# Performance work log

Measured on AMD Instinct MI355X. Metric: run time of the kernel, lower is better.

The kernel has to match this reference:

```python
import jax, jax.numpy as jnp
import numpy as np

NUM_HEADS = 6


def dwconv_tokens(tokens, H, W, w, b, stride):
    # tokens: (B, N, C) -> depthwise conv in (B, C, H, W) -> (B, N', C)
    B, N, C = tokens.shape
    x = tokens.transpose(0, 2, 1).reshape(B, C, H, W)
    y = jax.lax.conv_general_dilated(
        x, w, window_strides=(stride, stride), padding=[(1, 1), (1, 1)],
        feature_group_count=C, dimension_numbers=('NCHW', 'OIHW', 'NCHW'))
    y = y + b[None, :, None, None]
    Bc, Cc, Hs, Ws = y.shape
    return y.reshape(Bc, Cc, Hs * Ws).transpose(0, 2, 1), Hs, Ws


def neg_softmax(a):
    # sign(x) * softmax(|x|) along last axis
    return jnp.sign(a) * jax.nn.softmax(jnp.abs(a), axis=-1)


def split_heads(t, nh):
    B, N, C = t.shape
    return t.reshape(B, N, nh, C // nh).transpose(0, 2, 1, 3)  # (B, H, N, d)


def setup_inputs() -> dict:
    key = jax.random.key(0)
    ks = jax.random.split(key, 16)
    B, H, W, C = 8, 56, 56, 384
    N = H * W
    s = 0.02
    inp = {
        'x': jax.random.normal(ks[0], (B, N, C), jnp.float32),
        'H': H, 'W': W,
        'q_w': jax.random.normal(ks[1], (C, C), jnp.float32) * s,
        'q_b': jax.random.normal(ks[2], (C,), jnp.float32) * s,
        'k_w': jax.random.normal(ks[3], (C, C), jnp.float32) * s,
        'k_b': jax.random.normal(ks[4], (C,), jnp.float32) * s,
        'v_w': jax.random.normal(ks[5], (C, C), jnp.float32) * s,
        'v_b': jax.random.normal(ks[6], (C,), jnp.float32) * s,
        'q_dw_w': jax.random.normal(ks[7], (C, 1, 3, 3), jnp.float32) * 0.1,
        'q_dw_b': jax.random.normal(ks[8], (C,), jnp.float32) * s,
        'k_dw_w': jax.random.normal(ks[9], (C, 1, 3, 3), jnp.float32) * 0.1,
        'k_dw_b': jax.random.normal(ks[10], (C,), jnp.float32) * s,
        'v_dw_w': jax.random.normal(ks[11], (C, 1, 3, 3), jnp.float32) * 0.1,
        'v_dw_b': jax.random.normal(ks[12], (C,), jnp.float32) * s,
        'proj_w': jax.random.normal(ks[13], (C, C), jnp.float32) * s,
        'proj_b': jax.random.normal(ks[14], (C,), jnp.float32) * s,
    }
    return inp


def reference(x, H, W, q_w, q_b, k_w, k_b, v_w, v_b,
              q_dw_w, q_dw_b, k_dw_w, k_dw_b, v_dw_w, v_dw_b,
              proj_w, proj_b):
    B, N, C = x.shape
    nh = NUM_HEADS
    hd = C // nh
    scale = hd ** -0.5
    # linear q/k/v (torch Linear: x @ W.T + b)
    q = x @ q_w.T + q_b
    k = x @ k_w.T + k_b
    v = x @ v_w.T + v_b
    # depthwise conv projections (q: stride 1, k/v: stride 2)
    q, Hq, Wq = dwconv_tokens(q, H, W, q_dw_w, q_dw_b, 1)
    k, _, _ = dwconv_tokens(k, H, W, k_dw_w, k_dw_b, 2)
    v, _, _ = dwconv_tokens(v, H, W, v_dw_w, v_dw_b, 2)
    q = split_heads(q, nh)  # (B, nh, Nq, hd)
    k = split_heads(k, nh)  # (B, nh, Nk, hd)
    v = split_heads(v, nh)
    attn = jnp.einsum('bhqd,bhkd->bhqk', q, k) * scale
    attn = neg_softmax(attn)
    out = jnp.einsum('bhqk,bhkd->bhqd', attn, v)
    out = out.transpose(0, 2, 1, 3).reshape(B, -1, C)
    out = out @ proj_w.T + proj_b
    return out
```

## Files before the change

kernel.cpp:

```cpp
#include <hip/hip_runtime.h>
#include <hip/hip_bf16.h>
#include <stdint.h>

typedef __attribute__((ext_vector_type(4))) float f32x4;
typedef __attribute__((ext_vector_type(8))) short s16x8;
typedef __attribute__((ext_vector_type(4))) short s16x4;
typedef __attribute__((ext_vector_type(8))) unsigned short u16x8;

#define NB 8
#define HH 56
#define WW0 56
#define NC 384
#define NQTOK (HH*WW0)
#define NKTOK 784
#define NHEAD 6
#define HDIM 64
#define QSCALE 0.18033688f

__device__ __forceinline__ float bf2f(unsigned short u) {
    union { unsigned int i; float f; } x; x.i = ((unsigned int)u) << 16; return x.f;
}
__device__ __forceinline__ unsigned short f2bf(float f) {
    union { float f; unsigned int i; } x; x.f = f;
    unsigned int r = x.i + 0x7FFFu + ((x.i >> 16) & 1u);
    return (unsigned short)(r >> 16);
}
__device__ __forceinline__ unsigned short f2bf_rn(float f) {
    union { float f; unsigned int i; } x; x.f = f;
    return (unsigned short)((x.i + 0x8000u) >> 16);
}

__global__ __launch_bounds__(256) void prep_all(
    const float* __restrict__ x,
    const float* __restrict__ qw, const float* __restrict__ kw,
    const float* __restrict__ vw, const float* __restrict__ pw,
    const float* __restrict__ qb, const float* __restrict__ kb,
    const float* __restrict__ vb, const float* __restrict__ pb,
    const float* __restrict__ qdw, const float* __restrict__ kdw, const float* __restrict__ vdw,
    unsigned short* __restrict__ xbf, unsigned short* __restrict__ wbf,
    float* __restrict__ wtab, float* __restrict__ ball)
{
    const int bid = blockIdx.x;
    const int t = threadIdx.x;
    if (bid < 4704) {
        int i = bid*256 + t;
        f32x4 a0 = *(const f32x4*)&x[(size_t)i*8];
        f32x4 a1 = *(const f32x4*)&x[(size_t)i*8 + 4];
        u16x8 p;
        #pragma unroll
        for (int j = 0; j < 4; ++j) { p[j] = f2bf(a0[j]); p[j+4] = f2bf(a1[j]); }
        *(u16x8*)&xbf[(size_t)i*8] = p;
    } else if (bid < 4992) {
        int i = (bid - 4704)*256 + t;
        int m = i / 18432;
        const float* s = (m==0) ? qw : ((m==1) ? kw : ((m==2) ? vw : pw));
        int r = i - m*18432;
        f32x4 a0 = *(const f32x4*)&s[(size_t)r*8];
        f32x4 a1 = *(const f32x4*)&s[(size_t)r*8 + 4];
        u16x8 p;
        #pragma unroll
        for (int j = 0; j < 4; ++j) { p[j] = f2bf(a0[j]); p[j+4] = f2bf(a1[j]); }
        *(u16x8*)&wbf[(size_t)i*8] = p;
    } else {
        int j = (bid - 4992)*256 + t;
        if (j < 3*9*NC) {
            int m = j / (9*NC); int r = j - m*(9*NC);
            int tap = r / NC; int c = r - tap*NC;
            const float* src = (m==0) ? qdw : ((m==1) ? kdw : vdw);
            wtab[j] = src[c*9 + tap];
        } else {
            int jj = j - 3*9*NC;
            if (jj < 4*NC) {
                int m = jj / NC, r = jj - m*NC;
                ball[jj] = ((m==0) ? qb : ((m==1) ? kb : ((m==2) ? vb : pb)))[r];
            }
        }
    }
}

template<bool OUT_F32>
__global__ __launch_bounds__(512) void gemm_bt_bf(
    const unsigned short* __restrict__ A,
    const unsigned short* __restrict__ Wall,
    const float* __restrict__ Ball,
    unsigned short* __restrict__ Oa, unsigned short* __restrict__ Ob, unsigned short* __restrict__ Oc,
    float* __restrict__ Of,
    int ntiles)
{
    __shared__ unsigned short lA[256*64];
    __shared__ unsigned short lW[128*64];
    char* lAb = (char*)lA;
    char* lWb = (char*)lW;
    const int bid = blockIdx.x;
    const int nt = bid % ntiles;
    const int mt = bid / ntiles;
    const int mat = nt / 3;
    const int ncol = nt - mat*3;
    const unsigned short* W = Wall + (size_t)mat*NC*NC;
    const float* Bsel = Ball + mat*NC;
    unsigned short* Osel = (mat==0) ? Oa : ((mat==1) ? Ob : Oc);
    const int Mbase = mt*256, Nbase = ncol*128;
    const int t = threadIdx.x;
    const int w = t >> 6, l = t & 63;
    const int wr = w >> 1, wc = w & 1;
    const int lr = l & 15, lg = l >> 4;
    const int swg = (lr & 7) << 4;

    f32x4 acc[4][4] = {};
    for (int kt = 0; kt < 6; ++kt) {
        __syncthreads();
        #pragma unroll
        for (int i = 0; i < 4; ++i) {
            int c = i*512 + t;
            int row = c >> 3, c8 = c & 7;
            int sdst = row*128 + ((c8*16) ^ ((row & 7) << 4));
            *(u16x8*)(lAb + sdst) = *(const u16x8*)&A[(size_t)(Mbase+row)*NC + kt*64 + c8*8];
        }
        #pragma unroll
        for (int i = 0; i < 2; ++i) {
            int c = i*512 + t;
            int row = c >> 3, c8 = c & 7;
            int sdst = row*128 + ((c8*16) ^ ((row & 7) << 4));
            *(u16x8*)(lWb + sdst) = *(const u16x8*)&W[(size_t)(Nbase+row)*NC + kt*64 + c8*8];
        }
        __syncthreads();
        #pragma unroll
        for (int kk = 0; kk < 2; ++kk) {
            s16x8 af[4], bfr[4];
            #pragma unroll
            for (int m = 0; m < 4; ++m)
                af[m] = *(const s16x8*)(lAb + (wr*64 + m*16 + lr)*128 + ((kk*64 + lg*16) ^ swg));
            #pragma unroll
            for (int n = 0; n < 4; ++n)
                bfr[n] = *(const s16x8*)(lWb + (wc*64 + n*16 + lr)*128 + ((kk*64 + lg*16) ^ swg));
            #pragma unroll
            for (int m = 0; m < 4; ++m)
                #pragma unroll
                for (int n = 0; n < 4; ++n)
                    acc[m][n] = __builtin_amdgcn_mfma_f32_16x16x32_bf16(af[m], bfr[n], acc[m][n], 0, 0, 0);
        }
    }
    #pragma unroll
    for (int n = 0; n < 4; ++n) {
        int col = Nbase + wc*64 + n*16 + lr;
        float bias = Bsel[col];
        #pragma unroll
        for (int m = 0; m < 4; ++m) {
            int row0 = Mbase + wr*64 + m*16 + lg*4;
            #pragma unroll
            for (int r = 0; r < 4; ++r) {
                float vv = acc[m][n][r] + bias;
                if (OUT_F32) Of[(size_t)(row0 + r)*NC + col] = vv;
                else Osel[(size_t)(row0 + r)*NC + col] = f2bf(vv);
            }
        }
    }
}

template<int S, int HO, int WO, bool SCALE, int MODE>
__device__ __forceinline__ void dwconv_body(
    int idx,
    const unsigned short* __restrict__ in,
    const float* __restrict__ wt9,
    const float* __restrict__ bias,
    unsigned short* __restrict__ outp)
{
    const int nc8 = NC/8;
    int c8 = idx % nc8; int rest = idx / nc8;
    int wo = rest % WO; rest /= WO;
    int ho = rest % HO; int b = rest / HO;
    int c0 = c8*8;
    f32x4 b0 = *(const f32x4*)&bias[c0];
    f32x4 b1 = *(const f32x4*)&bias[c0+4];
    float acc[8];
    #pragma unroll
    for (int j = 0; j < 4; ++j) { acc[j] = b0[j]; acc[j+4] = b1[j]; }
    #pragma unroll
    for (int kh = 0; kh < 3; ++kh) {
        int h = ho*S + kh - 1;
        if (h < 0 || h >= HH) continue;
        #pragma unroll
        for (int kw = 0; kw < 3; ++kw) {
            int ww = wo*S + kw - 1;
            if (ww < 0 || ww >= WW0) continue;
            int tap = kh*3 + kw;
            u16x8 xv = *(const u16x8*)&in[((size_t)b*(HH*WW0) + h*WW0 + ww)*NC + c0];
            f32x4 w0 = *(const f32x4*)&wt9[tap*NC + c0];
            f32x4 w1 = *(const f32x4*)&wt9[tap*NC + c0 + 4];
            #pragma unroll
            for (int j = 0; j < 4; ++j) {
                acc[j]   += bf2f(xv[j])   * w0[j];
                acc[j+4] += bf2f(xv[j+4]) * w1[j];
            }
        }
    }
    if (SCALE) {
        #pragma unroll
        for (int j = 0; j < 8; ++j) acc[j] *= QSCALE;
    }
    int tok = ho*WO + wo;
    int hh = c0 >> 6, d0 = c0 & 63;
    if (MODE == 0) {
        u16x8 ov;
        #pragma unroll
        for (int j = 0; j < 8; ++j) ov[j] = f2bf(acc[j]);
        *(u16x8*)&outp[((size_t)b*(HO*WO) + tok)*NC + c0] = ov;
    } else if (MODE == 1) {
        u16x8 ov;
        #pragma unroll
        for (int j = 0; j < 8; ++j) ov[j] = f2bf(acc[j]);
        *(u16x8*)&outp[((size_t)(b*NHEAD + hh)*(HO*WO) + tok)*HDIM + d0] = ov;
    } else {
        size_t base = ((size_t)(b*NHEAD + hh)*HDIM + d0)*(HO*WO) + tok;
        #pragma unroll
        for (int j = 0; j < 8; ++j)
            outp[base + (size_t)j*(HO*WO)] = f2bf(acc[j]);
    }
}

__global__ __launch_bounds__(256) void dwconv_kv(
    const unsigned short* __restrict__ preK, const unsigned short* __restrict__ preV,
    const float* __restrict__ wtK, const float* __restrict__ wtV,
    const float* __restrict__ biasK, const float* __restrict__ biasV,
    unsigned short* __restrict__ Kpk, unsigned short* __restrict__ Vt)
{
    const int bid = blockIdx.x;
    if (bid < 1176) {
        int idx = bid*256 + threadIdx.x;
        dwconv_body<2,28,28,false,1>(idx, preK, wtK, biasK, Kpk);
    } else {
        int idx = (bid-1176)*256 + threadIdx.x;
        dwconv_body<2,28,28,false,2>(idx, preV, wtV, biasV, Vt);
    }
}

__global__ __launch_bounds__(256) void dwconv_q(
    const unsigned short* __restrict__ in,
    const float* __restrict__ wt9, const float* __restrict__ bias,
    unsigned short* __restrict__ outp)
{
    int idx = blockIdx.x*256 + threadIdx.x;
    dwconv_body<1,56,56,true,0>(idx, in, wt9, bias, outp);
}

__global__ __launch_bounds__(256) void attn_fwd(
    const unsigned short* __restrict__ Q,
    const unsigned short* __restrict__ Kpk,
    const unsigned short* __restrict__ Vt,
    unsigned short* __restrict__ ctx)
{
    __shared__ unsigned short lK[2][4096];
    __shared__ unsigned short lV[2][4096];
    const int bid = blockIdx.x;
    const int xcd = bid & 7, slot = bid >> 3;
    const int bh = xcd*6 + slot/25;
    const int qt = slot % 25;
    const int b = bh / NHEAD, h = bh - b*NHEAD;
    const int t = threadIdx.x;
    const int w = t >> 6, l = t & 63;
    const int lq = l & 15, lg = l >> 4;
    const int wq0 = qt*128 + w*32;
    const int wq0c = (wq0 > NQTOK-32) ? (NQTOK-32) : wq0;

    const unsigned short* Qb = Q + ((size_t)b*NQTOK + wq0c + lq)*NC + h*HDIM;
    s16x8 qA[2][2];
    qA[0][0] = *(const s16x8*)&Qb[lg*8];
    qA[0][1] = *(const s16x8*)&Qb[32 + lg*8];
    qA[1][0] = *(const s16x8*)&Qb[16*NC + lg*8];
    qA[1][1] = *(const s16x8*)&Qb[16*NC + 32 + lg*8];

    const char* Kg = (const char*)(Kpk + (size_t)bh*NKTOK*HDIM);
    const char* Vg = (const char*)(Vt + (size_t)bh*HDIM*NKTOK);
    char* lKb = (char*)lK;
    char* lVb = (char*)lV;

    const int cr0 = t >> 3;
    const int cr1 = cr0 + 32;
    const int cc  = (t & 7) * 16;
    const int dst0 = cr0*128 + (cc ^ ((cr0 & 7) << 4));
    const int dst1 = cr1*128 + (cc ^ ((cr1 & 7) << 4));

    uint4 rk0, rk1, rv0, rv1;
    #define LOADT(kb) do { \
        rk0 = *(const uint4*)(Kg + (size_t)((kb) + cr0)*128 + cc); \
        rk1 = *(const uint4*)(Kg + (size_t)((kb) + cr1)*128 + cc); \
        rv0 = *(const uint4*)(Vg + (size_t)cr0*1568 + (kb)*2 + cc); \
        rv1 = *(const uint4*)(Vg + (size_t)cr1*1568 + (kb)*2 + cc); \
    } while(0)
    #define WRITET(buf) do { \
        *(uint4*)(lKb + (buf)*8192 + dst0) = rk0; \
        *(uint4*)(lKb + (buf)*8192 + dst1) = rk1; \
        *(uint4*)(lVb + (buf)*8192 + dst0) = rv0; \
        *(uint4*)(lVb + (buf)*8192 + dst1) = rv1; \
    } while(0)

    const int swc = (lq & 7) << 4;
    const int ck0 = (lg*16) ^ swc;
    const int ck1 = (64 + lg*16) ^ swc;

    float ls[2] = {0.f, 0.f};
    f32x4 oacc[2][4] = {};

    LOADT(0);
    WRITET(0);
    __syncthreads();

    for (int kt = 0; kt < 12; ++kt) {
        const int cur = kt & 1;
        if (kt < 11) LOADT((kt+1)*64);
        const char* Kl = lKb + cur*8192;
        const char* Vl = lVb + cur*8192;
        f32x4 st[2][4] = {};
        __builtin_amdgcn_s_setprio(1);
        #pragma unroll
        for (int kfr = 0; kfr < 4; ++kfr) {
            int rb = (kfr*16 + lq)*128;
            s16x8 kf0 = *(const s16x8*)(Kl + rb + ck0);
            s16x8 kf1 = *(const s16x8*)(Kl + rb + ck1);
            st[0][kfr] = __builtin_amdgcn_mfma_f32_16x16x32_bf16(kf0, qA[0][0], st[0][kfr], 0,0,0);
            st[0][kfr] = __builtin_amdgcn_mfma_f32_16x16x32_bf16(kf1, qA[0][1], st[0][kfr], 0,0,0);
            st[1][kfr] = __builtin_amdgcn_mfma_f32_16x16x32_bf16(kf0, qA[1][0], st[1][kfr], 0,0,0);
            st[1][kfr] = __builtin_amdgcn_mfma_f32_16x16x32_bf16(kf1, qA[1][1], st[1][kfr], 0,0,0);
        }
        __builtin_amdgcn_s_setprio(0);
        s16x4 pbv[2][4];
        #pragma unroll
        for (int qf = 0; qf < 2; ++qf) {
            float rs = 0.f;
            #pragma unroll
            for (int kfr = 0; kfr < 4; ++kfr)
                #pragma unroll
                for (int r = 0; r < 4; ++r) {
                    float s = st[qf][kfr][r];
                    float e = __builtin_amdgcn_exp2f(fabsf(s));
                    rs += e;
                    pbv[qf][kfr][r] = (short)f2bf_rn(copysignf(e, s));
                }
            ls[qf] += rs;
        }
        __builtin_amdgcn_s_setprio(1);
        #pragma unroll
        for (int ks = 0; ks < 4; ++ks)
            #pragma unroll
            for (int f = 0; f < 4; ++f) {
                int va = (f*16 + lq)*128 + ((ks*32 + lg*8) ^ swc);
                s16x4 vvf = *(const s16x4*)(Vl + va);
                oacc[0][f] = __builtin_amdgcn_mfma_f32_16x16x16bf16_1k(vvf, pbv[0][ks], oacc[0][f], 0,0,0);
                oacc[1][f] = __builtin_amdgcn_mfma_f32_16x16x16bf16_1k(vvf, pbv[1][ks], oacc[1][f], 0,0,0);
            }
        __builtin_amdgcn_s_setprio(0);
        if (kt < 11) {
            WRITET(cur ^ 1);
            __syncthreads();
        }
    }
    {
        const unsigned short* Kb2 = (const unsigned short*)Kg;
        const unsigned short* Vb2 = (const unsigned short*)Vg;
        const unsigned short* kr = &Kb2[(size_t)(768 + lq)*HDIM];
        s16x8 kf0 = *(const s16x8*)&kr[lg*8];
        s16x8 kf1 = *(const s16x8*)&kr[32 + lg*8];
        f32x4 st[2] = {};
        st[0] = __builtin_amdgcn_mfma_f32_16x16x32_bf16(kf0, qA[0][0], st[0], 0,0,0);
        st[0] = __builtin_amdgcn_mfma_f32_16x16x32_bf16(kf1, qA[0][1], st[0], 0,0,0);
        st[1] = __builtin_amdgcn_mfma_f32_16x16x32_bf16(kf0, qA[1][0], st[1], 0,0,0);
        st[1] = __builtin_amdgcn_mfma_f32_16x16x32_bf16(kf1, qA[1][1], st[1], 0,0,0);
        s16x4 vv[4];
        #pragma unroll
        for (int f = 0; f < 4; ++f)
            vv[f] = *(const s16x4*)&Vb2[(size_t)(f*16 + lq)*NKTOK + 768 + lg*4];
        s16x4 pbv[2];
        #pragma unroll
        for (int qf = 0; qf < 2; ++qf) {
            float rs = 0.f;
            #pragma unroll
            for (int r = 0; r < 4; ++r) {
                float s = st[qf][r];
                float e = __builtin_amdgcn_exp2f(fabsf(s));
                rs += e;
                pbv[qf][r] = (short)f2bf_rn(copysignf(e, s));
            }
            ls[qf] += rs;
        }
        #pragma unroll
        for (int f = 0; f < 4; ++f) {
            oacc[0][f] = __builtin_amdgcn_mfma_f32_16x16x16bf16_1k(vv[f], pbv[0], oacc[0][f], 0,0,0);
            oacc[1][f] = __builtin_amdgcn_mfma_f32_16x16x16bf16_1k(vv[f], pbv[1], oacc[1][f], 0,0,0);
        }
    }
    if (wq0 < NQTOK) {
        #pragma unroll
        for (int qf = 0; qf < 2; ++qf) {
            float lr2 = ls[qf];
            lr2 += __shfl_xor(lr2, 16);
            lr2 += __shfl_xor(lr2, 32);
            float inv = 1.f / lr2;
            unsigned short* cb = ctx + ((size_t)b*NQTOK + wq0 + qf*16 + lq)*NC + h*HDIM;
            #pragma unroll
            for (int f = 0; f < 4; ++f) {
                s16x4 o;
                #pragma unroll
                for (int r = 0; r < 4; ++r) o[r] = (short)f2bf(oacc[qf][f][r] * inv);
                *(s16x4*)&cb[f*16 + lg*4] = o;
            }
        }
    }
    #undef LOADT
    #undef WRITET
}

extern "C" void kernel_launch(void* const* d_in, const int* in_sizes, int n_in,
                              void* d_out, int out_size, void* d_ws, size_t ws_size,
                              hipStream_t stream)
{
    (void)in_sizes; (void)n_in; (void)out_size; (void)ws_size;
    const float* x      = (const float*)d_in[0];
    const float* q_w    = (const float*)d_in[3];
    const float* q_b    = (const float*)d_in[4];
    const float* k_w    = (const float*)d_in[5];
    const float* k_b    = (const float*)d_in[6];
    const float* v_w    = (const float*)d_in[7];
    const float* v_b    = (const float*)d_in[8];
    const float* q_dw_w = (const float*)d_in[9];
    const float* q_dw_b = (const float*)d_in[10];
    const float* k_dw_w = (const float*)d_in[11];
    const float* k_dw_b = (const float*)d_in[12];
    const float* v_dw_w = (const float*)d_in[13];
    const float* v_dw_b = (const float*)d_in[14];
    const float* proj_w = (const float*)d_in[15];
    const float* proj_b = (const float*)d_in[16];
    float* outf = (float*)d_out;
    unsigned short* ws  = (unsigned short*)d_ws;

    const size_t nQ  = (size_t)NB*NQTOK*NC;
    const size_t nKc = (size_t)NB*NKTOK*NC;
    unsigned short* preQ = ws;
    unsigned short* preK = ws + nQ;
    unsigned short* Kpk  = ws + 2*nQ;
    unsigned short* Vt   = Kpk + nKc;
    unsigned short* wbf  = Vt + nKc;
    float* wtab = (float*)(wbf + (size_t)4*NC*NC);
    float* ball = wtab + 3*9*NC;
    unsigned short* preV = (unsigned short*)d_out;
    unsigned short* Qc   = (unsigned short*)d_out;
    unsigned short* xbf  = ((unsigned short*)d_out) + nQ;
    unsigned short* ctx  = preK;

    prep_all<<<dim3(5039), dim3(256), 0, stream>>>(
        x, q_w, k_w, v_w, proj_w, q_b, k_b, v_b, proj_b,
        q_dw_w, k_dw_w, v_dw_w, xbf, wbf, wtab, ball);
    gemm_bt_bf<false><<<dim3(98*9), dim3(512), 0, stream>>>(
        xbf, wbf, ball, preQ, preK, preV, nullptr, 9);
    dwconv_kv<<<dim3(2352), dim3(256), 0, stream>>>(
        preK, preV, wtab + 1*9*NC, wtab + 2*9*NC, k_dw_b, v_dw_b, Kpk, Vt);
    dwconv_q<<<dim3(4704), dim3(256), 0, stream>>>(preQ, wtab + 0*9*NC, q_dw_b, Qc);
    attn_fwd<<<dim3(1200), dim3(256), 0, stream>>>(Qc, Kpk, Vt, ctx);
    gemm_bt_bf<true><<<dim3(98*3), dim3(512), 0, stream>>>(
        ctx, wbf + (size_t)3*NC*NC, ball + 3*NC, nullptr, nullptr, nullptr, outf, 3);
}
```

Before: 181.6 us.

## Use 32x32x16 MFMA in projection GEMM and pack bf16 pairs via perm

The linear projection GEMM moves from sixteen 16x16x32 MFMA accumulators per wave to four 32x32x16 MFMA tiles, with new LDS fragment addressing and a new output index mapping. This cuts LDS fragment loads per MFMA and uses the larger MFMA shape. Separately, the attention softmax now packs two rounded bf16 values into one register with a single v_perm instead of converting and inserting them one at a time. The new mapping must line up with the 32x32 accumulator layout, and the larger accumulators add register pressure.

```diff
diff --git a/kernel.cpp b/kernel.cpp
--- a/kernel.cpp
+++ b/kernel.cpp
@@ -3,6 +3,7 @@
 #include <stdint.h>
 
 typedef __attribute__((ext_vector_type(4))) float f32x4;
+typedef __attribute__((ext_vector_type(16))) float f32x16;
 typedef __attribute__((ext_vector_type(8))) short s16x8;
 typedef __attribute__((ext_vector_type(4))) short s16x4;
 typedef __attribute__((ext_vector_type(8))) unsigned short u16x8;
@@ -25,9 +26,10 @@
     unsigned int r = x.i + 0x7FFFu + ((x.i >> 16) & 1u);
     return (unsigned short)(r >> 16);
 }
-__device__ __forceinline__ unsigned short f2bf_rn(float f) {
-    union { float f; unsigned int i; } x; x.f = f;
-    return (unsigned short)((x.i + 0x8000u) >> 16);
+__device__ __forceinline__ unsigned int pack2bf(float lo, float hi) {
+    unsigned int li = __builtin_bit_cast(unsigned int, lo) + 0x8000u;
+    unsigned int hi2 = __builtin_bit_cast(unsigned int, hi) + 0x8000u;
+    return __builtin_amdgcn_perm(hi2, li, 0x07060302u);
 }
 
 __global__ __launch_bounds__(256) void prep_all(
@@ -103,10 +105,10 @@
     const int t = threadIdx.x;
     const int w = t >> 6, l = t & 63;
     const int wr = w >> 1, wc = w & 1;
-    const int lr = l & 15, lg = l >> 4;
-    const int swg = (lr & 7) << 4;
-
-    f32x4 acc[4][4] = {};
+    const int l31 = l & 31, lhi = l >> 5;
+    const int swz = (l & 7) << 4;
+
+    f32x16 acc00 = {}, acc01 = {}, acc10 = {}, acc11 = {};
     for (int kt = 0; kt < 6; ++kt) {
         __syncthreads();
         #pragma unroll
@@ -125,33 +127,32 @@
         }
         __syncthreads();
         #pragma unroll
-        for (int kk = 0; kk < 2; ++kk) {
-            s16x8 af[4], bfr[4];
-            #pragma unroll
-            for (int m = 0; m < 4; ++m)
-                af[m] = *(const s16x8*)(lAb + (wr*64 + m*16 + lr)*128 + ((kk*64 + lg*16) ^ swg));
-            #pragma unroll
-            for (int n = 0; n < 4; ++n)
-                bfr[n] = *(const s16x8*)(lWb + (wc*64 + n*16 + lr)*128 + ((kk*64 + lg*16) ^ swg));
-            #pragma unroll
-            for (int m = 0; m < 4; ++m)
-                #pragma unroll
-                for (int n = 0; n < 4; ++n)
-                    acc[m][n] = __builtin_amdgcn_mfma_f32_16x16x32_bf16(af[m], bfr[n], acc[m][n], 0, 0, 0);
+        for (int s = 0; s < 4; ++s) {
+            int kb = (s*32 + lhi*16) ^ swz;
+            s16x8 a0 = *(const s16x8*)(lAb + (wr*64 + l31)*128 + kb);
+            s16x8 a1 = *(const s16x8*)(lAb + (wr*64 + 32 + l31)*128 + kb);
+            s16x8 b0 = *(const s16x8*)(lWb + (wc*64 + l31)*128 + kb);
+            s16x8 b1 = *(const s16x8*)(lWb + (wc*64 + 32 + l31)*128 + kb);
+            acc00 = __builtin_amdgcn_mfma_f32_32x32x16_bf16(a0, b0, acc00, 0, 0, 0);
+            acc01 = __builtin_amdgcn_mfma_f32_32x32x16_bf16(a0, b1, acc01, 0, 0, 0);
+            acc10 = __builtin_amdgcn_mfma_f32_32x32x16_bf16(a1, b0, acc10, 0, 0, 0);
+            acc11 = __builtin_amdgcn_mfma_f32_32x32x16_bf16(a1, b1, acc11, 0, 0, 0);
         }
     }
     #pragma unroll
-    for (int n = 0; n < 4; ++n) {
-        int col = Nbase + wc*64 + n*16 + lr;
+    for (int fn = 0; fn < 2; ++fn) {
+        int col = Nbase + wc*64 + fn*32 + l31;
         float bias = Bsel[col];
         #pragma unroll
-        for (int m = 0; m < 4; ++m) {
-            int row0 = Mbase + wr*64 + m*16 + lg*4;
-            #pragma unroll
-            for (int r = 0; r < 4; ++r) {
-                float vv = acc[m][n][r] + bias;
-                if (OUT_F32) Of[(size_t)(row0 + r)*NC + col] = vv;
-                else Osel[(size_t)(row0 + r)*NC + col] = f2bf(vv);
+        for (int fm = 0; fm < 2; ++fm) {
+            const f32x16& ac = (fm==0) ? ((fn==0) ? acc00 : acc01)
+                                       : ((fn==0) ? acc10 : acc11);
+            #pragma unroll
+            for (int reg = 0; reg < 16; ++reg) {
+                int row = Mbase + wr*64 + fm*32 + (reg & 3) + 8*(reg >> 2) + 4*lhi;
+                float vv = ac[reg] + bias;
+                if (OUT_F32) Of[(size_t)row*NC + col] = vv;
+                else Osel[(size_t)row*NC + col] = f2bf(vv);
             }
         }
     }
@@ -328,14 +329,20 @@
         for (int qf = 0; qf < 2; ++qf) {
             float rs = 0.f;
             #pragma unroll
-            for (int kfr = 0; kfr < 4; ++kfr)
+            for (int kfr = 0; kfr < 4; ++kfr) {
+                float p[4];
                 #pragma unroll
                 for (int r = 0; r < 4; ++r) {
                     float s = st[qf][kfr][r];
                     float e = __builtin_amdgcn_exp2f(fabsf(s));
                     rs += e;
-                    pbv[qf][kfr][r] = (short)f2bf_rn(copysignf(e, s));
+                    p[r] = copysignf(e, s);
                 }
+                uint2 pu;
+                pu.x = pack2bf(p[0], p[1]);
+                pu.y = pack2bf(p[2], p[3]);
+                pbv[qf][kfr] = __builtin_bit_cast(s16x4, pu);
+            }
             ls[qf] += rs;
         }
         __builtin_amdgcn_s_setprio(1);
@@ -372,14 +379,18 @@
         s16x4 pbv[2];
         #pragma unroll
         for (int qf = 0; qf < 2; ++qf) {
-            float rs = 0.f;
+            float rs = 0.f, p[4];
             #pragma unroll
             for (int r = 0; r < 4; ++r) {
                 float s = st[qf][r];
                 float e = __builtin_amdgcn_exp2f(fabsf(s));
                 rs += e;
-                pbv[qf][r] = (short)f2bf_rn(copysignf(e, s));
-            }
+                p[r] = copysignf(e, s);
+            }
+            uint2 pu;
+            pu.x = pack2bf(p[0], p[1]);
+            pu.y = pack2bf(p[2], p[3]);
+            pbv[qf] = __builtin_bit_cast(s16x4, pu);
             ls[qf] += rs;
         }
         #pragma unroll
```

Result: no change. 184.8 us (+1.7%).
